# Kernel tuning notes

Hardware: AMD Instinct MI355X
Metric: run time of the kernel (lower is better)

The kernel has to match this reference:

```python
import jax, jax.numpy as jnp
import numpy as np
import math

B_SZ, L, D_MODEL = 2, 2048, 1024
D_STATE, D_CONV, EXPAND = 16, 4, 2
D_INNER = EXPAND * D_MODEL
DT_RANK = math.ceil(D_MODEL / 16)


def setup_inputs() -> dict:
    key = jax.random.key(0)
    ks = jax.random.split(key, 9)
    s = 0.02
    x = jax.random.normal(ks[0], (B_SZ, L, D_MODEL), jnp.float32)
    W_in = jax.random.normal(ks[1], (D_MODEL, 2 * D_INNER), jnp.float32) * s
    conv_w = jax.random.normal(ks[2], (D_INNER, D_CONV), jnp.float32) * 0.1
    conv_b = jax.random.normal(ks[3], (D_INNER,), jnp.float32) * s
    W_xproj = jax.random.normal(ks[4], (D_INNER, DT_RANK + 2 * D_STATE), jnp.float32) * s
    W_dt = jax.random.normal(ks[5], (DT_RANK, D_INNER), jnp.float32) * s
    # dt bias init so softplus(bias) is log-uniform in [dt_min, dt_max]
    dt_min, dt_max = 0.001, 0.1
    dt = jnp.exp(jax.random.uniform(ks[6], (D_INNER,)) * (math.log(dt_max) - math.log(dt_min)) + math.log(dt_min))
    dt = jnp.maximum(dt, 1e-4)
    b_dt = dt + jnp.log(-jnp.expm1(-dt))
    A_log = jnp.log(jnp.broadcast_to(jnp.arange(1, D_STATE + 1, dtype=jnp.float32), (D_INNER, D_STATE)))
    D = jnp.ones((D_INNER,), jnp.float32)
    W_out = jax.random.normal(ks[7], (D_INNER, D_MODEL), jnp.float32) * s
    return {"x": x, "W_in": W_in, "conv_w": conv_w, "conv_b": conv_b,
            "W_xproj": W_xproj, "W_dt": W_dt, "b_dt": b_dt,
            "A_log": A_log, "D": D, "W_out": W_out}


def _silu(v):
    return v * jax.nn.sigmoid(v)


def _mamba_fwd(x, W_in, conv_w, conv_b, W_xproj, W_dt, b_dt, A_log, D, W_out):
    B, Ls, _ = x.shape
    xz = x @ W_in                         # (B, L, 2*d_inner)
    xb, z = jnp.split(xz, 2, axis=-1)
    # causal depthwise conv1d (pad left d_conv-1, truncate to L)
    xp = jnp.pad(xb, ((0, 0), (D_CONV - 1, 0), (0, 0)))
    conv = conv_b
    acc = jnp.zeros_like(xb)
    for k in range(D_CONV):
        acc = acc + xp[:, k:k + Ls, :] * conv_w[:, k]
    xb = _silu(acc + conv_b)
    # input-dependent dt, B, C
    proj = xb @ W_xproj                   # (B, L, dt_rank + 2*d_state)
    dt_in = proj[..., :DT_RANK]
    Bm = proj[..., DT_RANK:DT_RANK + D_STATE]   # (B, L, d_state)
    Cm = proj[..., DT_RANK + D_STATE:]          # (B, L, d_state)
    dt = jax.nn.softplus(dt_in @ W_dt + b_dt)   # (B, L, d_inner)
    A = -jnp.exp(A_log)                         # (d_inner, d_state)

    def step(h, inp):
        x_t, dt_t, B_t, C_t = inp               # (B,d_inner),(B,d_inner),(B,s),(B,s)
        dA = jnp.exp(dt_t[:, :, None] * A)      # (B, d_inner, d_state)
        h = dA * h + (dt_t[:, :, None] * B_t[:, None, :]) * x_t[:, :, None]
        y_t = jnp.einsum('bds,bs->bd', h, C_t)
        return h, y_t

    h0 = jnp.zeros((B, D_INNER, D_STATE), xb.dtype)
    xs = (xb.swapaxes(0, 1), dt.swapaxes(0, 1), Bm.swapaxes(0, 1), Cm.swapaxes(0, 1))
    _, ys = jax.lax.scan(step, h0, xs)          # (L, B, d_inner)
    y = ys.swapaxes(0, 1) + D * xb
    y = y * _silu(z)
    return y @ W_out                            # (B, L, d_model)


def reference(x, W_in, conv_w, conv_b, W_xproj, W_dt, b_dt, A_log, D, W_out):
    return _mamba_fwd(x, W_in, conv_w, conv_b, W_xproj, W_dt, b_dt, A_log, D, W_out)
```

## Files before the change

### kernel.cpp

```cpp
#include <hip/hip_runtime.h>
#include <hip/hip_bf16.h>
#include <math.h>

#define BSZ 2
#define LSEQ 2048
#define DMODEL 1024
#define DSTATE 16
#define DCONV 4
#define DINNER 2048
#define DTRANK 64
#define NPROJ (DTRANK + 2 * DSTATE)
#define NC 32
#define LC 64
#define KS 4
#define KCH (DINNER / KS)

using short8 = __attribute__((ext_vector_type(8))) short;
using f32x4 = __attribute__((ext_vector_type(4))) float;
using u16x4 = __attribute__((ext_vector_type(4))) unsigned short;

__device__ __forceinline__ float silu_f(float v) {
    return v / (1.f + expf(-v));
}
__device__ __forceinline__ float softplus_f(float v) {
    return fmaxf(v, 0.f) + log1pf(expf(-fabsf(v)));
}
__device__ __forceinline__ unsigned short f2bf(float f) {
    unsigned u = __builtin_bit_cast(unsigned, f);
    u += 0x7fffu + ((u >> 16) & 1u);
    return (unsigned short)(u >> 16);
}
__device__ __forceinline__ float bf2f(unsigned short u) {
    unsigned x = ((unsigned)u) << 16;
    return __builtin_bit_cast(float, x);
}

__device__ __forceinline__ void gld_lds16(const unsigned short* g, unsigned short* l) {
    __builtin_amdgcn_global_load_lds(
        (const __attribute__((address_space(1))) unsigned int*)g,
        (__attribute__((address_space(3))) unsigned int*)l, 16, 0, 0);
}

__device__ __forceinline__ int xcd_swz(int wg, int nwg) {
    return (wg & 7) * (nwg >> 3) + (wg >> 3);
}

__global__ __launch_bounds__(256) void prep_kernel(
    const float* __restrict__ x, const float* __restrict__ W_in,
    const float* __restrict__ W_out, const float* __restrict__ W_xproj,
    const float* __restrict__ W_dt,
    unsigned short* __restrict__ xbf, unsigned short* __restrict__ WinT,
    unsigned short* __restrict__ WoutT, unsigned short* __restrict__ WxT,
    unsigned short* __restrict__ WdtT) {
    int bid = blockIdx.x;
    if (bid < 4096) {
        int i = bid * 256 + threadIdx.x;
        float4 v = reinterpret_cast<const float4*>(x)[i];
        u16x4 o = {f2bf(v.x), f2bf(v.y), f2bf(v.z), f2bf(v.w)};
        reinterpret_cast<u16x4*>(xbf)[i] = o;
        return;
    }
    bid -= 4096;
    if (bid < 1024 + 512) {
        const float* in;
        unsigned short* outp;
        int R, Cc, gx;
        if (bid < 1024) { in = W_in; outp = WinT; R = 1024; Cc = 4096; gx = 64; }
        else { bid -= 1024; in = W_out; outp = WoutT; R = 2048; Cc = 1024; gx = 16; }
        const int bx = bid % gx, by = bid / gx;
        __shared__ float t64[64][65];
        const int tx = threadIdx.x & 63, ty = threadIdx.x >> 6;
        const int c0 = bx * 64, r0 = by * 64;
#pragma unroll
        for (int i = 0; i < 16; i++)
            t64[ty + 4 * i][tx] = in[(size_t)(r0 + ty + 4 * i) * Cc + c0 + tx];
        __syncthreads();
#pragma unroll
        for (int i = 0; i < 16; i++) {
            int rr = ty + 4 * i;
            outp[(size_t)(c0 + rr) * R + r0 + tx] = f2bf(t64[tx][rr]);
        }
        return;
    }
    bid -= 1536;
    const float* in;
    unsigned short* outp;
    int R, Cc, gx;
    if (bid < 192) { in = W_xproj; outp = WxT; R = 2048; Cc = 96; gx = 3; }
    else { bid -= 192; in = W_dt; outp = WdtT; R = 64; Cc = 2048; gx = 64; }
    const int bx = bid % gx, by = bid / gx;
    __shared__ float t[32][33];
    const int tx = threadIdx.x & 31, ty = threadIdx.x >> 5;
    const int c0 = bx * 32, r0 = by * 32;
    for (int i = ty; i < 32; i += 8)
        t[i][tx] = in[(size_t)(r0 + i) * Cc + c0 + tx];
    __syncthreads();
    for (int i = ty; i < 32; i += 8)
        outp[(size_t)(c0 + i) * R + r0 + tx] = f2bf(t[tx][i]);
}

template <int EPI, typename CT>
__global__ __launch_bounds__(512, 4) void gemm_bm256(
    const unsigned short* __restrict__ A, const unsigned short* __restrict__ Bt,
    CT* __restrict__ C, CT* __restrict__ C2, int M, int N, int K) {
    __shared__ __align__(16) unsigned short As[2][8192];
    __shared__ __align__(16) unsigned short Bs[2][4096];
    const int tid = threadIdx.x;
    const int lane = tid & 63;
    const int w8 = tid >> 6;
    const int wm = w8 >> 1, wn = w8 & 1;
    const int nwg = gridDim.x * gridDim.y;
    const int wg = xcd_swz(blockIdx.y * gridDim.x + blockIdx.x, nwg);
    const int m0 = (wg / gridDim.x) * 256, n0 = (wg % gridDim.x) * 128;
    const int fr = lane & 15, kg = lane >> 4;
    const int kswz = ((kg ^ ((fr >> 1) & 3)) << 3);
    const int r0 = tid >> 2;
    const int d0 = tid * 8;
    const int cs8 = (((tid & 3) ^ ((tid >> 3) & 3)) << 3);
    const int nt = K / 32;

    f32x4 acc[4][4];
#pragma unroll
    for (int m = 0; m < 4; m++)
#pragma unroll
        for (int n = 0; n < 4; n++) acc[m][n] = (f32x4){0.f, 0.f, 0.f, 0.f};

#define STAGE(buf, k0)                                                           \
    {                                                                            \
        gld_lds16(&A[(size_t)(m0 + r0) * K + (k0) + cs8], &As[buf][d0]);         \
        gld_lds16(&A[(size_t)(m0 + 128 + r0) * K + (k0) + cs8],                  \
                  &As[buf][d0 + 4096]);                                          \
        gld_lds16(&Bt[(size_t)(n0 + r0) * K + (k0) + cs8], &Bs[buf][d0]);        \
    }

    STAGE(0, 0);
    __syncthreads();

    int cur = 0;
    for (int t = 0; t < nt; t++) {
        if (t + 1 < nt) STAGE(cur ^ 1, (t + 1) * 32);
        short8 a[4], b[4];
#pragma unroll
        for (int m = 0; m < 4; m++)
            a[m] = *reinterpret_cast<const short8*>(
                &As[cur][(wm * 64 + m * 16 + fr) * 32 + kswz]);
#pragma unroll
        for (int n = 0; n < 4; n++)
            b[n] = *reinterpret_cast<const short8*>(
                &Bs[cur][(wn * 64 + n * 16 + fr) * 32 + kswz]);
#pragma unroll
        for (int m = 0; m < 4; m++)
#pragma unroll
            for (int n = 0; n < 4; n++)
                acc[m][n] = __builtin_amdgcn_mfma_f32_16x16x32_bf16(
                    a[m], b[n], acc[m][n], 0, 0, 0);
        __syncthreads();
        cur ^= 1;
    }
#undef STAGE

    const int g4 = kg * 4;
#pragma unroll
    for (int m = 0; m < 4; m++)
#pragma unroll
        for (int n = 0; n < 4; n++)
#pragma unroll
            for (int j = 0; j < 4; j++) {
                int mm = m0 + wm * 64 + m * 16 + g4 + j;
                int nn = n0 + wn * 64 + n * 16 + fr;
                float v = acc[m][n][j];
                if (EPI == 1) {
                    if (nn < DINNER)
                        C[(size_t)mm * DINNER + nn] = f2bf(v);
                    else
                        C2[(size_t)mm * DINNER + (nn - DINNER)] = f2bf(silu_f(v));
                } else {
                    if constexpr (sizeof(CT) == 2)
                        C[(size_t)mm * N + nn] = f2bf(v);
                    else
                        C[(size_t)mm * N + nn] = v;
                }
            }
}

template <int BN, typename CT>
__global__ __launch_bounds__(256) void gemm_mfma(
    const unsigned short* __restrict__ A, const unsigned short* __restrict__ Bt,
    CT* __restrict__ C, int M, int N, int K) {
    constexpr int NF = BN / 32;
    __shared__ __align__(16) unsigned short As[2][4096];
    __shared__ __align__(16) unsigned short Bs[2][BN * 32];
    const int tid = threadIdx.x;
    const int lane = tid & 63;
    const int wid = tid >> 6;
    const int wr = wid >> 1, wc = wid & 1;
    const int nwg = gridDim.x * gridDim.y;
    const int wg = xcd_swz(blockIdx.y * gridDim.x + blockIdx.x, nwg);
    const int m0 = (wg / gridDim.x) * 128, n0 = (wg % gridDim.x) * BN;

    const int r0 = tid >> 2;
    const int r1 = r0 + 64;
    const int d0 = tid * 8;
    const int d1 = d0 + 2048;
    const int cs8 = (((tid & 3) ^ ((tid >> 3) & 3)) << 3);

    f32x4 acc[4][NF];
#pragma unroll
    for (int m = 0; m < 4; m++)
#pragma unroll
        for (int n = 0; n < NF; n++) acc[m][n] = (f32x4){0.f, 0.f, 0.f, 0.f};

    const int fr = lane & 15;
    const int kg = lane >> 4;
    const int kswz = ((kg ^ ((fr >> 1) & 3)) << 3);
    const int nt = K / 32;

    gld_lds16(&A[(size_t)(m0 + r0) * K + cs8], &As[0][d0]);
    gld_lds16(&A[(size_t)(m0 + r1) * K + cs8], &As[0][d1]);
    gld_lds16(&Bt[(size_t)(n0 + r0) * K + cs8], &Bs[0][d0]);
    if constexpr (BN == 128)
        gld_lds16(&Bt[(size_t)(n0 + r1) * K + cs8], &Bs[0][d1]);
    __syncthreads();

    int cur = 0;
    for (int t = 0; t < nt; t++) {
        if (t + 1 < nt) {
            const int k0 = (t + 1) * 32;
            gld_lds16(&A[(size_t)(m0 + r0) * K + k0 + cs8], &As[cur ^ 1][d0]);
            gld_lds16(&A[(size_t)(m0 + r1) * K + k0 + cs8], &As[cur ^ 1][d1]);
            gld_lds16(&Bt[(size_t)(n0 + r0) * K + k0 + cs8], &Bs[cur ^ 1][d0]);
            if constexpr (BN == 128)
                gld_lds16(&Bt[(size_t)(n0 + r1) * K + k0 + cs8], &Bs[cur ^ 1][d1]);
        }
        short8 a[4], b[NF];
#pragma unroll
        for (int m = 0; m < 4; m++)
            a[m] = *reinterpret_cast<const short8*>(
                &As[cur][(wr * 64 + m * 16 + fr) * 32 + kswz]);
#pragma unroll
        for (int n = 0; n < NF; n++)
            b[n] = *reinterpret_cast<const short8*>(
                &Bs[cur][(wc * (BN / 2) + n * 16 + fr) * 32 + kswz]);
#pragma unroll
        for (int m = 0; m < 4; m++)
#pragma unroll
            for (int n = 0; n < NF; n++)
                acc[m][n] = __builtin_amdgcn_mfma_f32_16x16x32_bf16(
                    a[m], b[n], acc[m][n], 0, 0, 0);
        __syncthreads();
        cur ^= 1;
    }

    const int g4 = (lane >> 4) * 4;
#pragma unroll
    for (int m = 0; m < 4; m++)
#pragma unroll
        for (int n = 0; n < NF; n++)
#pragma unroll
            for (int j = 0; j < 4; j++) {
                int mm = m0 + wr * 64 + m * 16 + g4 + j;
                int nn = n0 + wc * (BN / 2) + n * 16 + fr;
                float v = acc[m][n][j];
                if constexpr (sizeof(CT) == 2)
                    C[(size_t)mm * N + nn] = f2bf(v);
                else
                    C[(size_t)mm * N + nn] = v;
            }
}

__global__ __launch_bounds__(256) void dt_gemm(
    const unsigned short* __restrict__ dtin,
    const unsigned short* __restrict__ WdtT,
    const float* __restrict__ bias,
    unsigned short* __restrict__ dtout) {
    const int lane = threadIdx.x & 63;
    const int wid = threadIdx.x >> 6;
    const int mt = wid >> 1, nh = wid & 1;
    const int m0 = blockIdx.x * 32;
    const int n0 = blockIdx.y * 128 + nh * 64;
    const int fr = lane & 15, kg = lane >> 4;

    f32x4 acc[4];
#pragma unroll
    for (int i = 0; i < 4; i++) acc[i] = (f32x4){0.f, 0.f, 0.f, 0.f};

#pragma unroll
    for (int step = 0; step < 2; step++) {
        short8 a = *reinterpret_cast<const short8*>(
            &dtin[(size_t)(m0 + mt * 16 + fr) * DTRANK + step * 32 + kg * 8]);
#pragma unroll
        for (int nt = 0; nt < 4; nt++) {
            short8 b = *reinterpret_cast<const short8*>(
                &WdtT[(size_t)(n0 + nt * 16 + fr) * DTRANK + step * 32 + kg * 8]);
            acc[nt] = __builtin_amdgcn_mfma_f32_16x16x32_bf16(a, b, acc[nt], 0, 0, 0);
        }
    }
    const int g4 = kg * 4;
#pragma unroll
    for (int nt = 0; nt < 4; nt++)
#pragma unroll
        for (int j = 0; j < 4; j++) {
            int m = m0 + mt * 16 + g4 + j;
            int n = n0 + nt * 16 + fr;
            dtout[(size_t)m * DINNER + n] = f2bf(softplus_f(acc[nt][j] + bias[n]));
        }
}

__global__ __launch_bounds__(256) void proj_conv(
    const unsigned short* __restrict__ xbpre, const float* __restrict__ w,
    const float* __restrict__ bconv, const unsigned short* __restrict__ WxT,
    unsigned short* __restrict__ xb_out, float* __restrict__ pp) {
    __shared__ __align__(16) unsigned short xbs[32][520];
    const int mb = blockIdx.x, kc = blockIdx.y;
    const int m0 = mb * 32;
    const int D0 = kc * KCH;

    {
        const int tcol = threadIdx.x & 63;
        const int trow = threadIdx.x >> 6;
        const int dd = D0 + tcol * 8;
        float wk0[8], wk1[8], wk2[8], wk3[8], bb[8];
#pragma unroll
        for (int q = 0; q < 8; q++) {
            float4 wv = *reinterpret_cast<const float4*>(&w[(dd + q) * 4]);
            wk0[q] = wv.x; wk1[q] = wv.y; wk2[q] = wv.z; wk3[q] = wv.w;
        }
        {
            float4 b0 = *reinterpret_cast<const float4*>(&bconv[dd]);
            float4 b1 = *reinterpret_cast<const float4*>(&bconv[dd + 4]);
            bb[0] = b0.x; bb[1] = b0.y; bb[2] = b0.z; bb[3] = b0.w;
            bb[4] = b1.x; bb[5] = b1.y; bb[6] = b1.z; bb[7] = b1.w;
        }
        const int rbase = m0 + trow * 8;
        const int tloc0 = rbase & (LSEQ - 1);
        float xm3[8], xm2[8], xm1[8];
        if (tloc0 >= 3) {
            short8 v3 = *reinterpret_cast<const short8*>(&xbpre[(size_t)(rbase - 3) * DINNER + dd]);
            short8 v2 = *reinterpret_cast<const short8*>(&xbpre[(size_t)(rbase - 2) * DINNER + dd]);
            short8 v1 = *reinterpret_cast<const short8*>(&xbpre[(size_t)(rbase - 1) * DINNER + dd]);
#pragma unroll
            for (int q = 0; q < 8; q++) {
                xm3[q] = bf2f((unsigned short)v3[q]);
                xm2[q] = bf2f((unsigned short)v2[q]);
                xm1[q] = bf2f((unsigned short)v1[q]);
            }
        } else {
#pragma unroll
            for (int q = 0; q < 8; q++) { xm3[q] = 0.f; xm2[q] = 0.f; xm1[q] = 0.f; }
        }
#pragma unroll
        for (int rr = 0; rr < 8; rr++) {
            short8 vc = *reinterpret_cast<const short8*>(
                &xbpre[(size_t)(rbase + rr) * DINNER + dd]);
            float xc[8];
            short8 o;
#pragma unroll
            for (int q = 0; q < 8; q++) {
                xc[q] = bf2f((unsigned short)vc[q]);
                float a = bb[q];
                a = fmaf(wk0[q], xm3[q], a);
                a = fmaf(wk1[q], xm2[q], a);
                a = fmaf(wk2[q], xm1[q], a);
                a = fmaf(wk3[q], xc[q], a);
                o[q] = (short)f2bf(silu_f(a));
            }
            *reinterpret_cast<short8*>(&xbs[trow * 8 + rr][tcol * 8]) = o;
            *reinterpret_cast<short8*>(
                &xb_out[(size_t)(rbase + rr) * DINNER + dd]) = o;
#pragma unroll
            for (int q = 0; q < 8; q++) { xm3[q] = xm2[q]; xm2[q] = xm1[q]; xm1[q] = xc[q]; }
        }
    }
    __syncthreads();

    const int lane = threadIdx.x & 63;
    const int wid = threadIdx.x >> 6;
    const int mt = wid >> 1;
    const int nh = wid & 1;
    const int fr = lane & 15;
    const int kg = lane >> 4;

    f32x4 acc[3];
#pragma unroll
    for (int i = 0; i < 3; i++) acc[i] = (f32x4){0.f, 0.f, 0.f, 0.f};

    for (int step = 0; step < KCH / 32; step++) {
        short8 a = *reinterpret_cast<const short8*>(
            &xbs[mt * 16 + fr][step * 32 + kg * 8]);
#pragma unroll
        for (int nt = 0; nt < 3; nt++) {
            int nrow = nh * 48 + nt * 16 + fr;
            short8 b = *reinterpret_cast<const short8*>(
                &WxT[(size_t)nrow * DINNER + D0 + step * 32 + kg * 8]);
            acc[nt] = __builtin_amdgcn_mfma_f32_16x16x32_bf16(a, b, acc[nt], 0, 0, 0);
        }
    }
    const int g4 = kg * 4;
#pragma unroll
    for (int nt = 0; nt < 3; nt++)
#pragma unroll
        for (int j = 0; j < 4; j++) {
            int m = m0 + mt * 16 + g4 + j;
            int n = nh * 48 + nt * 16 + fr;
            pp[((size_t)kc * (BSZ * LSEQ) + m) * NPROJ + n] = acc[nt][j];
        }
}

__global__ __launch_bounds__(256) void proj_reduce(
    const float* __restrict__ pp, float* __restrict__ proj,
    unsigned short* __restrict__ dtin) {
    int i = blockIdx.x * 256 + threadIdx.x;
    if (i >= BSZ * LSEQ * NPROJ) return;
    float s = 0.f;
#pragma unroll
    for (int kc = 0; kc < KS; kc++)
        s += pp[(size_t)kc * BSZ * LSEQ * NPROJ + i];
    proj[i] = s;
    int m = i / NPROJ;
    int n = i - m * NPROJ;
    if (n < DTRANK) dtin[(size_t)m * DTRANK + n] = f2bf(s);
}

__global__ __launch_bounds__(256) void scan_pass1(
    const unsigned short* __restrict__ xb, const unsigned short* __restrict__ dt,
    const float* __restrict__ proj, const float* __restrict__ A_log,
    float* __restrict__ aprod, float* __restrict__ hend) {
    __shared__ __align__(16) float Bsh[LC][DSTATE];
    const int tg = blockIdx.x * 256 + threadIdx.x;
    const int d = tg & (DINNER - 1);
    const int bc = tg >> 11;
    const int c = bc & (NC - 1);
    const int b = bc >> 5;

    for (int idx = threadIdx.x; idx < LC * DSTATE; idx += 256) {
        int ti = idx >> 4, j = idx & 15;
        Bsh[ti][j] = proj[(size_t)(b * LSEQ + c * LC + ti) * NPROJ + DTRANK + j];
    }
    __syncthreads();

    float Av[DSTATE], h[DSTATE], ap[DSTATE];
#pragma unroll
    for (int s = 0; s < DSTATE; s++) {
        Av[s] = -expf(A_log[d * DSTATE + s]);
        h[s] = 0.f;
        ap[s] = 1.f;
    }

    for (int i = 0; i < LC; i++) {
        size_t base = (size_t)(b * LSEQ + c * LC + i) * DINNER + d;
        float dtv = bf2f(dt[base]);
        float xv = bf2f(xb[base]);
        float dx = dtv * xv;
        float Bv[DSTATE];
        *reinterpret_cast<float4*>(&Bv[0])  = *reinterpret_cast<const float4*>(&Bsh[i][0]);
        *reinterpret_cast<float4*>(&Bv[4])  = *reinterpret_cast<const float4*>(&Bsh[i][4]);
        *reinterpret_cast<float4*>(&Bv[8])  = *reinterpret_cast<const float4*>(&Bsh[i][8]);
        *reinterpret_cast<float4*>(&Bv[12]) = *reinterpret_cast<const float4*>(&Bsh[i][12]);
#pragma unroll
        for (int s = 0; s < DSTATE; s++) {
            float dA = __expf(dtv * Av[s]);
            ap[s] *= dA;
            h[s] = fmaf(dA, h[s], dx * Bv[s]);
        }
    }

    size_t o = ((size_t)bc * DINNER + d) * DSTATE;
#pragma unroll
    for (int q = 0; q < 4; q++) {
        *reinterpret_cast<float4*>(&aprod[o + q * 4]) =
            make_float4(ap[4 * q], ap[4 * q + 1], ap[4 * q + 2], ap[4 * q + 3]);
        *reinterpret_cast<float4*>(&hend[o + q * 4]) =
            make_float4(h[4 * q], h[4 * q + 1], h[4 * q + 2], h[4 * q + 3]);
    }
}

__global__ __launch_bounds__(256) void scan_pass2(
    float* __restrict__ aprod, const float* __restrict__ hend) {
    const int tg = blockIdx.x * 256 + threadIdx.x;
    const int s = tg & (DSTATE - 1);
    const int d = (tg >> 4) & (DINNER - 1);
    const int b = tg >> 15;
    float h = 0.f;
    for (int c = 0; c < NC; c++) {
        size_t o = ((size_t)((b * NC + c) * DINNER) + d) * DSTATE + s;
        float a = aprod[o];
        float e = hend[o];
        aprod[o] = h;
        h = fmaf(a, h, e);
    }
}

__global__ __launch_bounds__(256) void scan_pass3(
    const unsigned short* __restrict__ xb, const unsigned short* __restrict__ dt,
    const float* __restrict__ proj, const float* __restrict__ hstart,
    const float* __restrict__ A_log, const float* __restrict__ Dp,
    const unsigned short* __restrict__ sz, unsigned short* __restrict__ ybf) {
    __shared__ __align__(16) float Bsh[LC][DSTATE];
    __shared__ __align__(16) float Csh[LC][DSTATE];
    const int tg = blockIdx.x * 256 + threadIdx.x;
    const int d = tg & (DINNER - 1);
    const int bc = tg >> 11;
    const int c = bc & (NC - 1);
    const int b = bc >> 5;

    for (int idx = threadIdx.x; idx < LC * 2 * DSTATE; idx += 256) {
        int ti = idx >> 5, j = idx & 31;
        float v = proj[(size_t)(b * LSEQ + c * LC + ti) * NPROJ + DTRANK + j];
        if (j < DSTATE) Bsh[ti][j] = v;
        else            Csh[ti][j - DSTATE] = v;
    }
    __syncthreads();

    float Av[DSTATE], h[DSTATE];
    size_t o = ((size_t)bc * DINNER + d) * DSTATE;
#pragma unroll
    for (int q = 0; q < 4; q++) {
        float4 hv = *reinterpret_cast<const float4*>(&hstart[o + q * 4]);
        h[4 * q] = hv.x; h[4 * q + 1] = hv.y; h[4 * q + 2] = hv.z; h[4 * q + 3] = hv.w;
    }
#pragma unroll
    for (int s = 0; s < DSTATE; s++)
        Av[s] = -expf(A_log[d * DSTATE + s]);
    const float Dd = Dp[d];

    for (int i = 0; i < LC; i++) {
        size_t base = (size_t)(b * LSEQ + c * LC + i) * DINNER + d;
        float dtv = bf2f(dt[base]);
        float xv = bf2f(xb[base]);
        float szv = bf2f(sz[base]);
        float dx = dtv * xv;
        float Bv[DSTATE], Cv[DSTATE];
        *reinterpret_cast<float4*>(&Bv[0])  = *reinterpret_cast<const float4*>(&Bsh[i][0]);
        *reinterpret_cast<float4*>(&Bv[4])  = *reinterpret_cast<const float4*>(&Bsh[i][4]);
        *reinterpret_cast<float4*>(&Bv[8])  = *reinterpret_cast<const float4*>(&Bsh[i][8]);
        *reinterpret_cast<float4*>(&Bv[12]) = *reinterpret_cast<const float4*>(&Bsh[i][12]);
        *reinterpret_cast<float4*>(&Cv[0])  = *reinterpret_cast<const float4*>(&Csh[i][0]);
        *reinterpret_cast<float4*>(&Cv[4])  = *reinterpret_cast<const float4*>(&Csh[i][4]);
        *reinterpret_cast<float4*>(&Cv[8])  = *reinterpret_cast<const float4*>(&Csh[i][8]);
        *reinterpret_cast<float4*>(&Cv[12]) = *reinterpret_cast<const float4*>(&Csh[i][12]);
        float p = 0.f;
#pragma unroll
        for (int s = 0; s < DSTATE; s++) {
            float dA = __expf(dtv * Av[s]);
            h[s] = fmaf(dA, h[s], dx * Bv[s]);
            p = fmaf(h[s], Cv[s], p);
        }
        ybf[base] = f2bf((p + Dd * xv) * szv);
    }
}

extern "C" void kernel_launch(void* const* d_in, const int* in_sizes, int n_in,
                              void* d_out, int out_size, void* d_ws,
                              size_t ws_size, hipStream_t stream) {
    const float* x = (const float*)d_in[0];
    const float* W_in = (const float*)d_in[1];
    const float* conv_w = (const float*)d_in[2];
    const float* conv_b = (const float*)d_in[3];
    const float* W_xproj = (const float*)d_in[4];
    const float* W_dt = (const float*)d_in[5];
    const float* b_dt = (const float*)d_in[6];
    const float* A_log = (const float*)d_in[7];
    const float* Dp = (const float*)d_in[8];
    const float* W_out = (const float*)d_in[9];
    float* out = (float*)d_out;

    char* ws = (char*)d_ws;
    const size_t MB = 1u << 20;
    float* pp    = (float*)(ws);
    float* aprod = (float*)(ws);
    float* hend  = (float*)(ws + 8 * MB);
    unsigned short* xbpre_bf = (unsigned short*)(ws + 16 * MB);
    unsigned short* ybf      = (unsigned short*)(ws + 16 * MB);
    unsigned short* sz_bf    = (unsigned short*)(ws + 32 * MB);
    unsigned short* xb_bf    = (unsigned short*)(ws + 48 * MB);
    unsigned short* dt_bf    = (unsigned short*)(ws + 64 * MB);
    float* projbuf           = (float*)(ws + 88 * MB);
    unsigned short* dtin_bf  = (unsigned short*)(ws + 90 * MB);
    unsigned short* xbf      = (unsigned short*)(ws + 91 * MB);
    unsigned short* WinT     = (unsigned short*)(ws + 99 * MB);
    unsigned short* WoutT    = (unsigned short*)(ws + 107 * MB);
    unsigned short* WxT      = (unsigned short*)(ws + 111 * MB);
    unsigned short* WdtT     = (unsigned short*)(ws + 112 * MB);

    const int M = BSZ * LSEQ;
    dim3 blk(256);

    prep_kernel<<<dim3(4096 + 1024 + 512 + 192 + 128), blk, 0, stream>>>(
        x, W_in, W_out, W_xproj, W_dt, xbf, WinT, WoutT, WxT, WdtT);

    gemm_bm256<1, unsigned short><<<dim3((2 * DINNER) / 128, M / 256), dim3(512),
                                    0, stream>>>(
        xbf, WinT, xbpre_bf, sz_bf, M, 2 * DINNER, DMODEL);

    proj_conv<<<dim3(M / 32, KS), blk, 0, stream>>>(
        xbpre_bf, conv_w, conv_b, WxT, xb_bf, pp);
    proj_reduce<<<dim3((M * NPROJ) / 256), blk, 0, stream>>>(pp, projbuf, dtin_bf);

    dt_gemm<<<dim3(M / 32, DINNER / 128), blk, 0, stream>>>(
        dtin_bf, WdtT, b_dt, dt_bf);

    const int nthreads1 = BSZ * NC * DINNER;
    scan_pass1<<<dim3(nthreads1 / 256), blk, 0, stream>>>(
        xb_bf, dt_bf, projbuf, A_log, aprod, hend);
    const int nthreads2 = BSZ * DINNER * DSTATE;
    scan_pass2<<<dim3(nthreads2 / 256), blk, 0, stream>>>(aprod, hend);
    scan_pass3<<<dim3(nthreads1 / 256), blk, 0, stream>>>(
        xb_bf, dt_bf, projbuf, aprod, A_log, Dp, sz_bf, ybf);

    gemm_mfma<64, float><<<dim3(DMODEL / 64, M / 128), blk, 0, stream>>>(
        ybf, WoutT, out, M, DMODEL, DINNER);
}
```

Baseline: 249.2 us.

## Fuse three scan passes into one cooperative kernel with grid syncs

Merges the chunked scan's three kernels (local chunk scan, cross-chunk carry propagation, final output pass) into a single cooperative launch of 512 blocks separated by grid-wide barriers. Each block caches the packed dt/x bf16 values for its chunk in shared memory (64 KB) during the first phase so the third phase does not re-read them from global memory, and the A coefficients stay in registers across phases. This removes two kernel launches and a duplicate global read, at the cost of grid-sync overhead, a large shared-memory footprint that limits occupancy, and a middle phase where only part of the grid does any work.

```diff
diff --git a/kernel.cpp b/kernel.cpp
--- a/kernel.cpp
+++ b/kernel.cpp
@@ -1,6 +1,9 @@
 #include <hip/hip_runtime.h>
 #include <hip/hip_bf16.h>
+#include <hip/hip_cooperative_groups.h>
 #include <math.h>
+
+namespace cg = cooperative_groups;
 
 #define BSZ 2
 #define LSEQ 2048
@@ -421,20 +424,30 @@
     if (n < DTRANK) dtin[(size_t)m * DTRANK + n] = f2bf(s);
 }
 
-__global__ __launch_bounds__(256) void scan_pass1(
+__global__ __launch_bounds__(256) void scan_fused(
     const unsigned short* __restrict__ xb, const unsigned short* __restrict__ dt,
     const float* __restrict__ proj, const float* __restrict__ A_log,
-    float* __restrict__ aprod, float* __restrict__ hend) {
-    __shared__ __align__(16) float Bsh[LC][DSTATE];
-    const int tg = blockIdx.x * 256 + threadIdx.x;
-    const int d = tg & (DINNER - 1);
-    const int bc = tg >> 11;
+    const float* __restrict__ Dp, const unsigned short* __restrict__ sz,
+    float* __restrict__ aprod, float* __restrict__ hend,
+    unsigned short* __restrict__ ybf) {
+    extern __shared__ __align__(16) char smem[];
+    unsigned int* dxs = (unsigned int*)smem;
+    float* Bsh = (float*)(smem + LC * 256 * 4);
+    float* Csh = Bsh + LC * DSTATE;
+
+    cg::grid_group grid = cg::this_grid();
+
+    const int tid = threadIdx.x;
+    const int bc = blockIdx.x >> 3;
     const int c = bc & (NC - 1);
     const int b = bc >> 5;
-
-    for (int idx = threadIdx.x; idx < LC * DSTATE; idx += 256) {
-        int ti = idx >> 4, j = idx & 15;
-        Bsh[ti][j] = proj[(size_t)(b * LSEQ + c * LC + ti) * NPROJ + DTRANK + j];
+    const int d = ((blockIdx.x & 7) << 8) + tid;
+
+    for (int idx = tid; idx < LC * 2 * DSTATE; idx += 256) {
+        int ti = idx >> 5, j = idx & 31;
+        float v = proj[(size_t)(b * LSEQ + c * LC + ti) * NPROJ + DTRANK + j];
+        if (j < DSTATE) Bsh[ti * DSTATE + j] = v;
+        else            Csh[ti * DSTATE + (j - DSTATE)] = v;
     }
     __syncthreads();
 
@@ -448,22 +461,19 @@
 
     for (int i = 0; i < LC; i++) {
         size_t base = (size_t)(b * LSEQ + c * LC + i) * DINNER + d;
-        float dtv = bf2f(dt[base]);
-        float xv = bf2f(xb[base]);
+        unsigned short dtb = dt[base];
+        unsigned short xbb = xb[base];
+        dxs[i * 256 + tid] = ((unsigned)dtb << 16) | (unsigned)xbb;
+        float dtv = bf2f(dtb);
+        float xv = bf2f(xbb);
         float dx = dtv * xv;
-        float Bv[DSTATE];
-        *reinterpret_cast<float4*>(&Bv[0])  = *reinterpret_cast<const float4*>(&Bsh[i][0]);
-        *reinterpret_cast<float4*>(&Bv[4])  = *reinterpret_cast<const float4*>(&Bsh[i][4]);
-        *reinterpret_cast<float4*>(&Bv[8])  = *reinterpret_cast<const float4*>(&Bsh[i][8]);
-        *reinterpret_cast<float4*>(&Bv[12]) = *reinterpret_cast<const float4*>(&Bsh[i][12]);
 #pragma unroll
         for (int s = 0; s < DSTATE; s++) {
             float dA = __expf(dtv * Av[s]);
             ap[s] *= dA;
-            h[s] = fmaf(dA, h[s], dx * Bv[s]);
-        }
-    }
-
+            h[s] = fmaf(dA, h[s], dx * Bsh[i * DSTATE + s]);
+        }
+    }
     size_t o = ((size_t)bc * DINNER + d) * DSTATE;
 #pragma unroll
     for (int q = 0; q < 4; q++) {
@@ -472,78 +482,47 @@
         *reinterpret_cast<float4*>(&hend[o + q * 4]) =
             make_float4(h[4 * q], h[4 * q + 1], h[4 * q + 2], h[4 * q + 3]);
     }
-}
-
-__global__ __launch_bounds__(256) void scan_pass2(
-    float* __restrict__ aprod, const float* __restrict__ hend) {
-    const int tg = blockIdx.x * 256 + threadIdx.x;
-    const int s = tg & (DSTATE - 1);
-    const int d = (tg >> 4) & (DINNER - 1);
-    const int b = tg >> 15;
-    float h = 0.f;
-    for (int c = 0; c < NC; c++) {
-        size_t o = ((size_t)((b * NC + c) * DINNER) + d) * DSTATE + s;
-        float a = aprod[o];
-        float e = hend[o];
-        aprod[o] = h;
-        h = fmaf(a, h, e);
-    }
-}
-
-__global__ __launch_bounds__(256) void scan_pass3(
-    const unsigned short* __restrict__ xb, const unsigned short* __restrict__ dt,
-    const float* __restrict__ proj, const float* __restrict__ hstart,
-    const float* __restrict__ A_log, const float* __restrict__ Dp,
-    const unsigned short* __restrict__ sz, unsigned short* __restrict__ ybf) {
-    __shared__ __align__(16) float Bsh[LC][DSTATE];
-    __shared__ __align__(16) float Csh[LC][DSTATE];
-    const int tg = blockIdx.x * 256 + threadIdx.x;
-    const int d = tg & (DINNER - 1);
-    const int bc = tg >> 11;
-    const int c = bc & (NC - 1);
-    const int b = bc >> 5;
-
-    for (int idx = threadIdx.x; idx < LC * 2 * DSTATE; idx += 256) {
-        int ti = idx >> 5, j = idx & 31;
-        float v = proj[(size_t)(b * LSEQ + c * LC + ti) * NPROJ + DTRANK + j];
-        if (j < DSTATE) Bsh[ti][j] = v;
-        else            Csh[ti][j - DSTATE] = v;
-    }
-    __syncthreads();
-
-    float Av[DSTATE], h[DSTATE];
-    size_t o = ((size_t)bc * DINNER + d) * DSTATE;
+    __threadfence();
+    grid.sync();
+
+    {
+        const int tg2 = blockIdx.x * 256 + tid;
+        if (tg2 < BSZ * DINNER * DSTATE) {
+            const int s2 = tg2 & (DSTATE - 1);
+            const int d2 = (tg2 >> 4) & (DINNER - 1);
+            const int b2 = tg2 >> 15;
+            float hh = 0.f;
+            for (int c2 = 0; c2 < NC; c2++) {
+                size_t o2 = ((size_t)((b2 * NC + c2) * DINNER) + d2) * DSTATE + s2;
+                float a = aprod[o2];
+                float e = hend[o2];
+                aprod[o2] = hh;
+                hh = fmaf(a, hh, e);
+            }
+        }
+    }
+    __threadfence();
+    grid.sync();
+
 #pragma unroll
     for (int q = 0; q < 4; q++) {
-        float4 hv = *reinterpret_cast<const float4*>(&hstart[o + q * 4]);
+        float4 hv = *reinterpret_cast<const float4*>(&aprod[o + q * 4]);
         h[4 * q] = hv.x; h[4 * q + 1] = hv.y; h[4 * q + 2] = hv.z; h[4 * q + 3] = hv.w;
     }
-#pragma unroll
-    for (int s = 0; s < DSTATE; s++)
-        Av[s] = -expf(A_log[d * DSTATE + s]);
     const float Dd = Dp[d];
-
     for (int i = 0; i < LC; i++) {
         size_t base = (size_t)(b * LSEQ + c * LC + i) * DINNER + d;
-        float dtv = bf2f(dt[base]);
-        float xv = bf2f(xb[base]);
+        unsigned v = dxs[i * 256 + tid];
+        float dtv = bf2f((unsigned short)(v >> 16));
+        float xv = bf2f((unsigned short)(v & 0xffffu));
         float szv = bf2f(sz[base]);
         float dx = dtv * xv;
-        float Bv[DSTATE], Cv[DSTATE];
-        *reinterpret_cast<float4*>(&Bv[0])  = *reinterpret_cast<const float4*>(&Bsh[i][0]);
-        *reinterpret_cast<float4*>(&Bv[4])  = *reinterpret_cast<const float4*>(&Bsh[i][4]);
-        *reinterpret_cast<float4*>(&Bv[8])  = *reinterpret_cast<const float4*>(&Bsh[i][8]);
-        *reinterpret_cast<float4*>(&Bv[12]) = *reinterpret_cast<const float4*>(&Bsh[i][12]);
-        *reinterpret_cast<float4*>(&Cv[0])  = *reinterpret_cast<const float4*>(&Csh[i][0]);
-        *reinterpret_cast<float4*>(&Cv[4])  = *reinterpret_cast<const float4*>(&Csh[i][4]);
-        *reinterpret_cast<float4*>(&Cv[8])  = *reinterpret_cast<const float4*>(&Csh[i][8]);
-        *reinterpret_cast<float4*>(&Cv[12]) = *reinterpret_cast<const float4*>(&Csh[i][12]);
         float p = 0.f;
 #pragma unroll
         for (int s = 0; s < DSTATE; s++) {
             float dA = __expf(dtv * Av[s]);
-            h[s] = fmaf(dA, h[s], dx * Bv[s]);
-            p = fmaf(h[s], Cv[s], p);
+            h[s] = fmaf(dA, h[s], dx * Bsh[i * DSTATE + s]);
+            p = fmaf(h[s], Csh[i * DSTATE + s], p);
         }
         ybf[base] = f2bf((p + Dd * xv) * szv);
     }
@@ -599,13 +578,14 @@
     dt_gemm<<<dim3(M / 32, DINNER / 128), blk, 0, stream>>>(
         dtin_bf, WdtT, b_dt, dt_bf);
 
-    const int nthreads1 = BSZ * NC * DINNER;
-    scan_pass1<<<dim3(nthreads1 / 256), blk, 0, stream>>>(
-        xb_bf, dt_bf, projbuf, A_log, aprod, hend);
-    const int nthreads2 = BSZ * DINNER * DSTATE;
-    scan_pass2<<<dim3(nthreads2 / 256), blk, 0, stream>>>(aprod, hend);
-    scan_pass3<<<dim3(nthreads1 / 256), blk, 0, stream>>>(
-        xb_bf, dt_bf, projbuf, aprod, A_log, Dp, sz_bf, ybf);
+    {
+        void* kargs[] = {(void*)&xb_bf, (void*)&dt_bf, (void*)&projbuf,
+                         (void*)&A_log, (void*)&Dp, (void*)&sz_bf,
+                         (void*)&aprod, (void*)&hend, (void*)&ybf};
+        hipLaunchCooperativeKernel((const void*)scan_fused, dim3(512), dim3(256),
+                                   kargs, LC * 256 * 4 + 2 * LC * DSTATE * 4,
+                                   stream);
+    }
 
     gemm_mfma<64, float><<<dim3(DMODEL / 64, M / 128), blk, 0, stream>>>(
         ybf, WoutT, out, M, DMODEL, DINNER);
```

Result: slower. 514.5 us (+106.4%).
